# Kernel tuning notes

Hardware: AMD Instinct MI355X
Metric: run time of the kernel (lower is better)

Reference implementation:

```python
import jax, jax.numpy as jnp
import numpy as np
import math

NUM_HEADS = 8
EMB = 256

def setup_inputs() -> dict:
    key = jax.random.key(0)
    ks = jax.random.split(key, 9)
    B_, N, C = 1024, 64, EMB  # 16 images * 64 windows, 8x8 window, C=256
    nW = 64
    q = jax.random.normal(ks[0], (B_, N, C), dtype=jnp.float32)
    k = jax.random.normal(ks[1], (B_, N, C), dtype=jnp.float32)
    v = jax.random.normal(ks[2], (B_, N, C), dtype=jnp.float32)
    mask = jax.random.normal(ks[3], (nW, N, N), dtype=jnp.float32)
    # MLP params (Linear: y = x @ W^T + b; we store W already transposed for x @ W)
    hid = 4 * C
    s1 = 1.0 / math.sqrt(C)
    s2 = 1.0 / math.sqrt(hid)
    w1 = jax.random.uniform(ks[4], (C, hid), minval=-s1, maxval=s1, dtype=jnp.float32)
    b1 = jax.random.uniform(ks[5], (hid,), minval=-s1, maxval=s1, dtype=jnp.float32)
    w2 = jax.random.uniform(ks[6], (hid, C), minval=-s2, maxval=s2, dtype=jnp.float32)
    b2 = jax.random.uniform(ks[7], (C,), minval=-s2, maxval=s2, dtype=jnp.float32)
    return {"q": q, "k": k, "v": v, "mask": mask, "H": 64, "W": 64,
            "w1": w1, "b1": b1, "w2": w2, "b2": b2}

def reference(q, k, v, mask, H, W, w1, b1, w2, b2):
    B_, N, C = q.shape
    h = NUM_HEADS
    d = C // h
    # separate heads: (B_, h, N, d)
    qh = q.reshape(B_, N, h, d).transpose(0, 2, 1, 3)
    kh = k.reshape(B_, N, h, d).transpose(0, 2, 1, 3)
    vh = v.reshape(B_, N, h, d).transpose(0, 2, 1, 3)
    attn = jnp.einsum('bhnd,bhmd->bhnm', qh, kh)  # raw scores
    nW = mask.shape[0]
    # additive window mask BEFORE scaling (faithful to original order)
    attn = attn.reshape(B_ // nW, nW, h, N, N) + mask[None, :, None, :, :]
    attn = attn.reshape(B_, h, N, N) / math.sqrt(d)
    attn = jax.nn.softmax(attn, axis=-1)
    out = jnp.einsum('bhnm,bhmd->bhnd', attn, vh)
    out = out.transpose(0, 2, 1, 3).reshape(B_, N, C)  # recombine heads
    # linear Mlp (dropout is identity at p=0.0); torch nn.GELU is exact erf
    hmid = jax.nn.gelu(out @ w1 + b1, approximate=False)
    out = out + (hmid @ w2 + b2)
    return out
```

## Files before the change

kernel.cpp:

```cpp
#include <hip/hip_runtime.h>
#include <hip/hip_bf16.h>
#include <cstdint>
#include <cstddef>

typedef __attribute__((ext_vector_type(8))) short bf16x8;
typedef __attribute__((ext_vector_type(4))) float f32x4;

static __device__ __forceinline__ unsigned short f2bf(float f) {
    union { float f; unsigned int u; } x; x.f = f;
    unsigned int u = x.u;
    unsigned int r = (u + 0x7FFFu + ((u >> 16) & 1u)) >> 16;
    return (unsigned short)r;
}

static __device__ __forceinline__ f32x4 mfma_bf16(bf16x8 a, bf16x8 b, f32x4 c) {
    return __builtin_amdgcn_mfma_f32_16x16x32_bf16(a, b, c, 0, 0, 0);
}

static __device__ __forceinline__ bf16x8 pack8(float4 a, float4 b) {
    bf16x8 f;
    f[0]=(short)f2bf(a.x); f[1]=(short)f2bf(a.y); f[2]=(short)f2bf(a.z); f[3]=(short)f2bf(a.w);
    f[4]=(short)f2bf(b.x); f[5]=(short)f2bf(b.y); f[6]=(short)f2bf(b.z); f[7]=(short)f2bf(b.w);
    return f;
}

static __device__ __forceinline__ float gelu_erf(float v) {
    float s = v * 0.70710678118654752f;
    float a = fabsf(s);
    float t = __builtin_amdgcn_rcpf(1.0f + 0.3275911f * a);
    float poly = ((((1.061405429f * t - 1.453152027f) * t + 1.421413741f) * t
                   - 0.284496736f) * t + 0.254829592f) * t;
    float e = 1.0f - poly * __expf(-a * a);
    float erfv = copysignf(e, s);
    return 0.5f * v * (1.0f + erfv);
}

static __device__ __forceinline__ void load_lds16(const unsigned short* g, unsigned short* l) {
    __builtin_amdgcn_global_load_lds(
        (const __attribute__((address_space(1))) unsigned int*)g,
        (__attribute__((address_space(3))) unsigned int*)l, 16, 0, 0);
}

__global__ __launch_bounds__(256) void attn_kernel(
    const float* __restrict__ q, const float* __restrict__ k,
    const float* __restrict__ v, const float* __restrict__ mask,
    float* __restrict__ xout)
{
    __shared__ unsigned short Qs[64][40];
    __shared__ unsigned short Ks[64][40];
    __shared__ unsigned short Vt[32][72];
    __shared__ unsigned short Ps[64][72];

    const int tid  = threadIdx.x;
    const int b    = blockIdx.x >> 3;
    const int h    = blockIdx.x & 7;
    const int lane = tid & 63;
    const int l15  = lane & 15;
    const int g    = lane >> 4;
    const int w    = tid >> 6;

    {
        int row = tid >> 2;
        int seg = tid & 3;
        size_t base = ((size_t)(b * 64 + row)) * 256 + h * 32 + seg * 8;

        float4 a0 = *(const float4*)(q + base);
        float4 a1 = *(const float4*)(q + base + 4);
        unsigned short* p = &Qs[row][seg * 8];
        p[0]=f2bf(a0.x); p[1]=f2bf(a0.y); p[2]=f2bf(a0.z); p[3]=f2bf(a0.w);
        p[4]=f2bf(a1.x); p[5]=f2bf(a1.y); p[6]=f2bf(a1.z); p[7]=f2bf(a1.w);

        a0 = *(const float4*)(k + base);
        a1 = *(const float4*)(k + base + 4);
        p = &Ks[row][seg * 8];
        p[0]=f2bf(a0.x); p[1]=f2bf(a0.y); p[2]=f2bf(a0.z); p[3]=f2bf(a0.w);
        p[4]=f2bf(a1.x); p[5]=f2bf(a1.y); p[6]=f2bf(a1.z); p[7]=f2bf(a1.w);

        a0 = *(const float4*)(v + base);
        a1 = *(const float4*)(v + base + 4);
        int c = seg * 8;
        Vt[c + 0][row] = f2bf(a0.x);
        Vt[c + 1][row] = f2bf(a0.y);
        Vt[c + 2][row] = f2bf(a0.z);
        Vt[c + 3][row] = f2bf(a0.w);
        Vt[c + 4][row] = f2bf(a1.x);
        Vt[c + 5][row] = f2bf(a1.y);
        Vt[c + 6][row] = f2bf(a1.z);
        Vt[c + 7][row] = f2bf(a1.w);
    }
    __syncthreads();

    f32x4 s[4];
    {
        bf16x8 aQ = *(const bf16x8*)&Qs[w * 16 + l15][g * 8];
        #pragma unroll
        for (int ct = 0; ct < 4; ++ct) {
            bf16x8 bK = *(const bf16x8*)&Ks[ct * 16 + l15][g * 8];
            f32x4 z = {0.f, 0.f, 0.f, 0.f};
            s[ct] = mfma_bf16(aQ, bK, z);
        }
    }

    const float* mbase = mask + (size_t)(b & 63) * 4096;
    const float INV = 0.17677669529663688f;
    float rsum[4];
    #pragma unroll
    for (int r = 0; r < 4; ++r) {
        int row = w * 16 + g * 4 + r;
        float pr[4];
        #pragma unroll
        for (int ct = 0; ct < 4; ++ct)
            pr[ct] = (s[ct][r] + mbase[row * 64 + ct * 16 + l15]) * INV;
        float m = fmaxf(fmaxf(pr[0], pr[1]), fmaxf(pr[2], pr[3]));
        #pragma unroll
        for (int off = 1; off < 16; off <<= 1)
            m = fmaxf(m, __shfl_xor(m, off));
        float sum = 0.f;
        #pragma unroll
        for (int ct = 0; ct < 4; ++ct) { pr[ct] = __expf(pr[ct] - m); sum += pr[ct]; }
        #pragma unroll
        for (int off = 1; off < 16; off <<= 1)
            sum += __shfl_xor(sum, off);
        rsum[r] = sum;
        #pragma unroll
        for (int ct = 0; ct < 4; ++ct)
            Ps[row][ct * 16 + l15] = f2bf(pr[ct]);
    }

    f32x4 o[2] = {};
    #pragma unroll
    for (int ks = 0; ks < 2; ++ks) {
        bf16x8 pa = *(const bf16x8*)&Ps[w * 16 + l15][ks * 32 + g * 8];
        #pragma unroll
        for (int n = 0; n < 2; ++n) {
            bf16x8 vb = *(const bf16x8*)&Vt[n * 16 + l15][ks * 32 + g * 8];
            o[n] = mfma_bf16(pa, vb, o[n]);
        }
    }

    #pragma unroll
    for (int n = 0; n < 2; ++n) {
        #pragma unroll
        for (int r = 0; r < 4; ++r) {
            int row = w * 16 + g * 4 + r;
            xout[((size_t)(b * 64 + row)) * 256 + h * 32 + n * 16 + l15] =
                o[n][r] / rsum[r];
        }
    }
}

__global__ __launch_bounds__(256) void prep_w1(const float* __restrict__ src,
                                               unsigned short* __restrict__ dst)
{
    __shared__ float tile[64][65];
    const int kt = blockIdx.x, hc = blockIdx.y;
    const int t = threadIdx.x;
    const int r0 = t >> 4, c4 = (t & 15) * 4;
    #pragma unroll
    for (int p = 0; p < 4; ++p) {
        int kk = r0 + p * 16;
        float4 d = *(const float4*)(src + (size_t)(kt * 64 + kk) * 1024 + hc * 64 + c4);
        tile[kk][c4+0]=d.x; tile[kk][c4+1]=d.y; tile[kk][c4+2]=d.z; tile[kk][c4+3]=d.w;
    }
    __syncthreads();
    #pragma unroll
    for (int i = 0; i < 2; ++i) {
        int f = t + 256 * i;
        int wnh = f >> 8;
        int r   = f & 255;
        int ksl = r >> 7;
        int h2  = (r >> 6) & 1;
        int r3  = r & 63;
        int l15v = r3 >> 2, gv = r3 & 3;
        int n_local = wnh * 32 + h2 * 16 + l15v;
        int k_local = ksl * 32 + gv * 8;
        int ks = kt * 2 + ksl;
        unsigned short tmp[8];
        #pragma unroll
        for (int e = 0; e < 8; ++e) tmp[e] = f2bf(tile[k_local + e][n_local]);
        size_t off = (size_t)hc * 16384 + ((size_t)((wnh * 8 + ks) * 2 + h2)) * 512
                   + (gv * 16 + l15v) * 8;
        *(bf16x8*)(dst + off) = *(const bf16x8*)tmp;
    }
}

__global__ __launch_bounds__(256) void prep_w2(const float* __restrict__ src,
                                               unsigned short* __restrict__ dst)
{
    __shared__ float tile[64][65];
    const int wno = blockIdx.x, hc = blockIdx.y;
    const int t = threadIdx.x;
    const int r0 = t >> 4, c4 = (t & 15) * 4;
    #pragma unroll
    for (int p = 0; p < 4; ++p) {
        int kk = r0 + p * 16;
        float4 d = *(const float4*)(src + (size_t)(hc * 64 + kk) * 256 + wno * 64 + c4);
        tile[kk][c4+0]=d.x; tile[kk][c4+1]=d.y; tile[kk][c4+2]=d.z; tile[kk][c4+3]=d.w;
    }
    __syncthreads();
    #pragma unroll
    for (int i = 0; i < 2; ++i) {
        int f = t + 256 * i;
        int ks2 = f >> 8;
        int r   = f & 255;
        int tq  = r >> 6;
        int r3  = r & 63;
        int l15v = r3 >> 2, gv = r3 & 3;
        int c_local = tq * 16 + l15v;
        int k_local = ks2 * 32 + gv * 8;
        unsigned short tmp[8];
        #pragma unroll
        for (int e = 0; e < 8; ++e) tmp[e] = f2bf(tile[k_local + e][c_local]);
        size_t off = (size_t)hc * 16384 + ((size_t)((wno * 2 + ks2) * 4 + tq)) * 512
                   + (gv * 16 + l15v) * 8;
        *(bf16x8*)(dst + off) = *(const bf16x8*)tmp;
    }
}

__global__ __launch_bounds__(512, 2) void mlp_fused(
    const float* __restrict__ xin, float* __restrict__ xio,
    const unsigned short* __restrict__ wt1, const float* __restrict__ b1,
    const unsigned short* __restrict__ wt2, const float* __restrict__ b2)
{
    __shared__ unsigned short w1c[2][16384];
    __shared__ unsigned short w2c[2][16384];
    __shared__ unsigned short Hs[128][72];

    const int tid  = threadIdx.x;
    const int lane = tid & 63;
    const int l15  = lane & 15;
    const int g    = lane >> 4;
    const int wid  = tid >> 6;
    const int wmh  = wid >> 1, wnh = wid & 1;
    const int wmo  = wid >> 2, wno = wid & 3;
    const int fb   = (g * 16 + l15) * 8;

    const size_t rowbase = (size_t)blockIdx.x * 128;

    auto stage = [&](const unsigned short* gbase, unsigned short* lbase) {
        #pragma unroll
        for (int i = 0; i < 4; ++i) {
            load_lds16(gbase + (i * 512 + tid) * 8,
                       lbase + (i * 512 + wid * 64) * 8);
        }
    };

    stage(wt1, &w1c[0][0]);
    stage(wt2, &w2c[0][0]);

    bf16x8 xf[2][8];
    #pragma unroll
    for (int mt = 0; mt < 2; ++mt) {
        const float* xr = xin + (rowbase + wmh * 32 + mt * 16 + l15) * 256;
        #pragma unroll
        for (int ks = 0; ks < 8; ++ks) {
            float4 a0 = *(const float4*)(xr + ks * 32 + g * 8);
            float4 a1 = *(const float4*)(xr + ks * 32 + g * 8 + 4);
            xf[mt][ks] = pack8(a0, a1);
        }
    }

    f32x4 oacc[4][4] = {};

    for (int hc = 0; hc < 16; ++hc) {
        const int cur = hc & 1;
        __syncthreads();

        if (hc < 15) {
            stage(wt1 + (size_t)(hc + 1) * 16384, &w1c[cur ^ 1][0]);
            stage(wt2 + (size_t)(hc + 1) * 16384, &w2c[cur ^ 1][0]);
        }

        f32x4 hacc[2][2] = {};
        #pragma unroll
        for (int ks = 0; ks < 8; ++ks) {
            bf16x8 b0  = *(const bf16x8*)&w1c[cur][((wnh * 8 + ks) * 2 + 0) * 512 + fb];
            bf16x8 b1f = *(const bf16x8*)&w1c[cur][((wnh * 8 + ks) * 2 + 1) * 512 + fb];
            hacc[0][0] = mfma_bf16(xf[0][ks], b0,  hacc[0][0]);
            hacc[0][1] = mfma_bf16(xf[0][ks], b1f, hacc[0][1]);
            hacc[1][0] = mfma_bf16(xf[1][ks], b0,  hacc[1][0]);
            hacc[1][1] = mfma_bf16(xf[1][ks], b1f, hacc[1][1]);
        }

        bf16x8 bF[2][4];
        #pragma unroll
        for (int ks2 = 0; ks2 < 2; ++ks2)
            #pragma unroll
            for (int t = 0; t < 4; ++t)
                bF[ks2][t] = *(const bf16x8*)&w2c[cur][((wno * 2 + ks2) * 4 + t) * 512 + fb];

        #pragma unroll
        for (int nt = 0; nt < 2; ++nt) {
            int coll = wnh * 32 + nt * 16 + l15;
            float bias = b1[hc * 64 + coll];
            #pragma unroll
            for (int mt = 0; mt < 2; ++mt) {
                #pragma unroll
                for (int r = 0; r < 4; ++r) {
                    float vv = gelu_erf(hacc[mt][nt][r] + bias);
                    Hs[wmh * 32 + mt * 16 + g * 4 + r][coll] = f2bf(vv);
                }
            }
        }
        __syncthreads();

        #pragma unroll
        for (int ks2 = 0; ks2 < 2; ++ks2) {
            bf16x8 aF[4];
            #pragma unroll
            for (int t = 0; t < 4; ++t)
                aF[t] = *(const bf16x8*)&Hs[wmo * 64 + t * 16 + l15][ks2 * 32 + g * 8];
            #pragma unroll
            for (int mt = 0; mt < 4; ++mt)
                #pragma unroll
                for (int nt = 0; nt < 4; ++nt)
                    oacc[mt][nt] = mfma_bf16(aF[mt], bF[ks2][nt], oacc[mt][nt]);
        }
    }

    #pragma unroll
    for (int nt = 0; nt < 4; ++nt) {
        int col = wno * 64 + nt * 16 + l15;
        float bias = b2[col];
        #pragma unroll
        for (int mt = 0; mt < 4; ++mt) {
            #pragma unroll
            for (int r = 0; r < 4; ++r) {
                size_t idx = (rowbase + wmo * 64 + mt * 16 + g * 4 + r) * 256 + col;
                xio[idx] = oacc[mt][nt][r] + bias + xio[idx];
            }
        }
    }
}

extern "C" void kernel_launch(void* const* d_in, const int* in_sizes, int n_in,
                              void* d_out, int out_size, void* d_ws, size_t ws_size,
                              hipStream_t stream)
{
    const float* q    = (const float*)d_in[0];
    const float* k    = (const float*)d_in[1];
    const float* v    = (const float*)d_in[2];
    const float* mask = (const float*)d_in[3];
    const float* w1   = (const float*)d_in[6];
    const float* b1   = (const float*)d_in[7];
    const float* w2   = (const float*)d_in[8];
    const float* b2   = (const float*)d_in[9];

    float* xio = (float*)d_out;

    unsigned short* wt1 = (unsigned short*)d_ws;
    unsigned short* wt2 = wt1 + (size_t)1024 * 256;

    prep_w1<<<dim3(4, 16), 256, 0, stream>>>(w1, wt1);
    prep_w2<<<dim3(4, 16), 256, 0, stream>>>(w2, wt2);

    attn_kernel<<<8192, 256, 0, stream>>>(q, k, v, mask, xio);

    mlp_fused<<<512, 512, 0, stream>>>(xio, xio, wt1, b1, wt2, b2);
}
```

Baseline: 184.5 us.

## Halve MLP hidden chunk to 32 columns for smaller LDS and higher occupancy

```diff
diff --git a/kernel.cpp b/kernel.cpp
--- a/kernel.cpp
+++ b/kernel.cpp
@@ -7,10 +7,8 @@
 typedef __attribute__((ext_vector_type(4))) float f32x4;
 
 static __device__ __forceinline__ unsigned short f2bf(float f) {
-    union { float f; unsigned int u; } x; x.f = f;
-    unsigned int u = x.u;
-    unsigned int r = (u + 0x7FFFu + ((u >> 16) & 1u)) >> 16;
-    return (unsigned short)r;
+    __hip_bfloat16 h = __float2bfloat16(f);
+    return *reinterpret_cast<unsigned short*>(&h);
 }
 
 static __device__ __forceinline__ f32x4 mfma_bf16(bf16x8 a, bf16x8 b, f32x4 c) {
@@ -153,32 +151,32 @@
                                                unsigned short* __restrict__ dst)
 {
     __shared__ float tile[64][65];
-    const int kt = blockIdx.x, hc = blockIdx.y;
+    const int kt = blockIdx.x, nb = blockIdx.y;
     const int t = threadIdx.x;
     const int r0 = t >> 4, c4 = (t & 15) * 4;
     #pragma unroll
     for (int p = 0; p < 4; ++p) {
         int kk = r0 + p * 16;
-        float4 d = *(const float4*)(src + (size_t)(kt * 64 + kk) * 1024 + hc * 64 + c4);
+        float4 d = *(const float4*)(src + (size_t)(kt * 64 + kk) * 1024 + nb * 64 + c4);
         tile[kk][c4+0]=d.x; tile[kk][c4+1]=d.y; tile[kk][c4+2]=d.z; tile[kk][c4+3]=d.w;
     }
     __syncthreads();
     #pragma unroll
     for (int i = 0; i < 2; ++i) {
         int f = t + 256 * i;
-        int wnh = f >> 8;
-        int r   = f & 255;
-        int ksl = r >> 7;
-        int h2  = (r >> 6) & 1;
-        int r3  = r & 63;
-        int l15v = r3 >> 2, gv = r3 & 3;
-        int n_local = wnh * 32 + h2 * 16 + l15v;
+        int ksl = f >> 8;
+        int ntg = (f >> 6) & 3;
+        int gv  = (f >> 4) & 3;
+        int l15v = f & 15;
+        int n_local = ntg * 16 + l15v;
         int k_local = ksl * 32 + gv * 8;
+        int c  = nb * 2 + (ntg >> 1);
+        int nt = ntg & 1;
         int ks = kt * 2 + ksl;
         unsigned short tmp[8];
         #pragma unroll
         for (int e = 0; e < 8; ++e) tmp[e] = f2bf(tile[k_local + e][n_local]);
-        size_t off = (size_t)hc * 16384 + ((size_t)((wnh * 8 + ks) * 2 + h2)) * 512
+        size_t off = (size_t)c * 8192 + (size_t)((ks * 2 + nt) * 512)
                    + (gv * 16 + l15v) * 8;
         *(bf16x8*)(dst + off) = *(const bf16x8*)tmp;
     }
@@ -188,50 +186,49 @@
                                                unsigned short* __restrict__ dst)
 {
     __shared__ float tile[64][65];
-    const int wno = blockIdx.x, hc = blockIdx.y;
+    const int ob = blockIdx.x, kb = blockIdx.y;
     const int t = threadIdx.x;
     const int r0 = t >> 4, c4 = (t & 15) * 4;
     #pragma unroll
     for (int p = 0; p < 4; ++p) {
         int kk = r0 + p * 16;
-        float4 d = *(const float4*)(src + (size_t)(hc * 64 + kk) * 256 + wno * 64 + c4);
+        float4 d = *(const float4*)(src + (size_t)(kb * 64 + kk) * 256 + ob * 64 + c4);
         tile[kk][c4+0]=d.x; tile[kk][c4+1]=d.y; tile[kk][c4+2]=d.z; tile[kk][c4+3]=d.w;
     }
     __syncthreads();
     #pragma unroll
     for (int i = 0; i < 2; ++i) {
         int f = t + 256 * i;
-        int ks2 = f >> 8;
-        int r   = f & 255;
-        int tq  = r >> 6;
-        int r3  = r & 63;
-        int l15v = r3 >> 2, gv = r3 & 3;
+        int ksl = f >> 8;
+        int tq  = (f >> 6) & 3;
+        int gv  = (f >> 4) & 3;
+        int l15v = f & 15;
         int c_local = tq * 16 + l15v;
-        int k_local = ks2 * 32 + gv * 8;
+        int k_local = ksl * 32 + gv * 8;
+        int c = kb * 2 + ksl;
         unsigned short tmp[8];
         #pragma unroll
         for (int e = 0; e < 8; ++e) tmp[e] = f2bf(tile[k_local + e][c_local]);
-        size_t off = (size_t)hc * 16384 + ((size_t)((wno * 2 + ks2) * 4 + tq)) * 512
+        size_t off = (size_t)c * 8192 + (size_t)((ob * 4 + tq) * 512)
                    + (gv * 16 + l15v) * 8;
         *(bf16x8*)(dst + off) = *(const bf16x8*)tmp;
     }
 }
 
-__global__ __launch_bounds__(512, 2) void mlp_fused(
+__global__ __launch_bounds__(512, 4) void mlp_fused(
     const float* __restrict__ xin, float* __restrict__ xio,
     const unsigned short* __restrict__ wt1, const float* __restrict__ b1,
     const unsigned short* __restrict__ wt2, const float* __restrict__ b2)
 {
-    __shared__ unsigned short w1c[2][16384];
-    __shared__ unsigned short w2c[2][16384];
-    __shared__ unsigned short Hs[128][72];
+    __shared__ unsigned short w1c[2][8192];
+    __shared__ unsigned short w2c[2][8192];
+    __shared__ unsigned short Hs[128][40];
 
     const int tid  = threadIdx.x;
     const int lane = tid & 63;
     const int l15  = lane & 15;
     const int g    = lane >> 4;
     const int wid  = tid >> 6;
-    const int wmh  = wid >> 1, wnh = wid & 1;
     const int wmo  = wid >> 2, wno = wid & 3;
     const int fb   = (g * 16 + l15) * 8;
 
@@ -239,7 +236,7 @@
 
     auto stage = [&](const unsigned short* gbase, unsigned short* lbase) {
         #pragma unroll
-        for (int i = 0; i < 4; ++i) {
+        for (int i = 0; i < 2; ++i) {
             load_lds16(gbase + (i * 512 + tid) * 8,
                        lbase + (i * 512 + wid * 64) * 8);
         }
@@ -248,74 +245,63 @@
     stage(wt1, &w1c[0][0]);
     stage(wt2, &w2c[0][0]);
 
-    bf16x8 xf[2][8];
-    #pragma unroll
-    for (int mt = 0; mt < 2; ++mt) {
-        const float* xr = xin + (rowbase + wmh * 32 + mt * 16 + l15) * 256;
+    bf16x8 xf[8];
+    {
+        const float* xr = xin + (rowbase + wid * 16 + l15) * 256;
         #pragma unroll
         for (int ks = 0; ks < 8; ++ks) {
             float4 a0 = *(const float4*)(xr + ks * 32 + g * 8);
             float4 a1 = *(const float4*)(xr + ks * 32 + g * 8 + 4);
-            xf[mt][ks] = pack8(a0, a1);
+            xf[ks] = pack8(a0, a1);
         }
     }
 
     f32x4 oacc[4][4] = {};
 
-    for (int hc = 0; hc < 16; ++hc) {
+    for (int hc = 0; hc < 32; ++hc) {
         const int cur = hc & 1;
         __syncthreads();
 
-        if (hc < 15) {
-            stage(wt1 + (size_t)(hc + 1) * 16384, &w1c[cur ^ 1][0]);
-            stage(wt2 + (size_t)(hc + 1) * 16384, &w2c[cur ^ 1][0]);
-        }
-
-        f32x4 hacc[2][2] = {};
+        if (hc < 31) {
+            stage(wt1 + (size_t)(hc + 1) * 8192, &w1c[cur ^ 1][0]);
+            stage(wt2 + (size_t)(hc + 1) * 8192, &w2c[cur ^ 1][0]);
+        }
+
+        f32x4 hacc[2] = {};
         #pragma unroll
         for (int ks = 0; ks < 8; ++ks) {
-            bf16x8 b0  = *(const bf16x8*)&w1c[cur][((wnh * 8 + ks) * 2 + 0) * 512 + fb];
-            bf16x8 b1f = *(const bf16x8*)&w1c[cur][((wnh * 8 + ks) * 2 + 1) * 512 + fb];
-            hacc[0][0] = mfma_bf16(xf[0][ks], b0,  hacc[0][0]);
-            hacc[0][1] = mfma_bf16(xf[0][ks], b1f, hacc[0][1]);
-            hacc[1][0] = mfma_bf16(xf[1][ks], b0,  hacc[1][0]);
-            hacc[1][1] = mfma_bf16(xf[1][ks], b1f, hacc[1][1]);
-        }
-
-        bf16x8 bF[2][4];
-        #pragma unroll
-        for (int ks2 = 0; ks2 < 2; ++ks2)
+            bf16x8 b0  = *(const bf16x8*)&w1c[cur][(ks * 2 + 0) * 512 + fb];
+            bf16x8 b1f = *(const bf16x8*)&w1c[cur][(ks * 2 + 1) * 512 + fb];
+            hacc[0] = mfma_bf16(xf[ks], b0,  hacc[0]);
+            hacc[1] = mfma_bf16(xf[ks], b1f, hacc[1]);
+        }
+
+        bf16x8 bF[4];
+        #pragma unroll
+        for (int t = 0; t < 4; ++t)
+            bF[t] = *(const bf16x8*)&w2c[cur][(wno * 4 + t) * 512 + fb];
+
+        #pragma unroll
+        for (int nt = 0; nt < 2; ++nt) {
+            int coll = nt * 16 + l15;
+            float bias = b1[hc * 32 + coll];
             #pragma unroll
-            for (int t = 0; t < 4; ++t)
-                bF[ks2][t] = *(const bf16x8*)&w2c[cur][((wno * 2 + ks2) * 4 + t) * 512 + fb];
-
-        #pragma unroll
-        for (int nt = 0; nt < 2; ++nt) {
-            int coll = wnh * 32 + nt * 16 + l15;
-            float bias = b1[hc * 64 + coll];
+            for (int r = 0; r < 4; ++r) {
+                float vv = gelu_erf(hacc[nt][r] + bias);
+                Hs[wid * 16 + g * 4 + r][coll] = f2bf(vv);
+            }
+        }
+        __syncthreads();
+
+        bf16x8 aF[4];
+        #pragma unroll
+        for (int t = 0; t < 4; ++t)
+            aF[t] = *(const bf16x8*)&Hs[wmo * 64 + t * 16 + l15][g * 8];
+        #pragma unroll
+        for (int mt = 0; mt < 4; ++mt)
             #pragma unroll
-            for (int mt = 0; mt < 2; ++mt) {
-                #pragma unroll
-                for (int r = 0; r < 4; ++r) {
-                    float vv = gelu_erf(hacc[mt][nt][r] + bias);
-                    Hs[wmh * 32 + mt * 16 + g * 4 + r][coll] = f2bf(vv);
-                }
-            }
-        }
-        __syncthreads();
-
-        #pragma unroll
-        for (int ks2 = 0; ks2 < 2; ++ks2) {
-            bf16x8 aF[4];
-            #pragma unroll
-            for (int t = 0; t < 4; ++t)
-                aF[t] = *(const bf16x8*)&Hs[wmo * 64 + t * 16 + l15][ks2 * 32 + g * 8];
-            #pragma unroll
-            for (int mt = 0; mt < 4; ++mt)
-                #pragma unroll
-                for (int nt = 0; nt < 4; ++nt)
-                    oacc[mt][nt] = mfma_bf16(aF[mt], bF[ks2][nt], oacc[mt][nt]);
-        }
+            for (int nt = 0; nt < 4; ++nt)
+                oacc[mt][nt] = mfma_bf16(aF[mt], bF[nt], oacc[mt][nt]);
     }
 
     #pragma unroll
```

New measurement: 184.6 us. About the same (+0.1%).
